# Performance work log

Measured on AMD Instinct MI355X. Metric: run time of the kernel, lower is better.

The kernel has to match this reference:

```python
import jax, jax.numpy as jnp
import numpy as np

BETA = 0.9
THRESH = 1.0
SLOPE = 25.0  # fast_sigmoid surrogate slope

@jax.custom_vjp
def spike(x):
    # forward: heaviside(mem - threshold); backward: fast-sigmoid surrogate
    return (x > 0).astype(x.dtype)

def _spike_fwd(x):
    return (x > 0).astype(x.dtype), x

def _spike_bwd(x, g):
    return (g / (SLOPE * jnp.abs(x) + 1.0) ** 2,)

spike.defvjp(_spike_fwd, _spike_bwd)

def lif_step(mem, cur):
    # snntorch Leaky, reset_mechanism='subtract': reset from previous mem (detached)
    reset = jax.lax.stop_gradient((mem > THRESH).astype(cur.dtype))
    mem_new = BETA * mem + cur - reset * THRESH
    spk = spike(mem_new - THRESH)
    return spk, mem_new

def setup_inputs() -> dict:
    key = jax.random.key(0)
    ks = jax.random.split(key, 10)
    B, S, T = 256, 8, 25
    A, V, H, E = 512, 512, 256, 128
    a_seq = (jax.random.uniform(ks[0], (B, S, T, A)) < 0.2).astype(jnp.float32)
    v_seq = (jax.random.uniform(ks[1], (B, S, T, V)) < 0.2).astype(jnp.float32)
    def lin(kw, kb, out_d, in_d):
        lim = 1.0 / np.sqrt(in_d)
        W = jax.random.uniform(kw, (out_d, in_d), minval=-lim, maxval=lim, dtype=jnp.float32)
        b = jax.random.uniform(kb, (out_d,), minval=-lim, maxval=lim, dtype=jnp.float32)
        return W, b
    W_a1, b_a1 = lin(ks[2], ks[3], H, A)
    W_a2, b_a2 = lin(ks[4], ks[5], E, H)
    W_v1, b_v1 = lin(ks[6], ks[7], H, V)
    W_v2, b_v2 = lin(ks[8], ks[9], E, H)
    return dict(a_seq=a_seq, v_seq=v_seq, W_a1=W_a1, b_a1=b_a1, W_a2=W_a2, b_a2=b_a2,
                W_v1=W_v1, b_v1=b_v1, W_v2=W_v2, b_v2=b_v2)

def reference(a_seq, v_seq, W_a1, b_a1, W_a2, b_a2, W_v1, b_v1, W_v2, b_v2):
    B, S, T, A = a_seq.shape
    V = v_seq.shape[-1]
    H = W_a1.shape[0]
    E = W_a2.shape[0]
    BS = B * S  # segments are independent -> fold into batch
    a = a_seq.reshape(BS, T, A).transpose(1, 0, 2)  # [T, BS, A]
    v = v_seq.reshape(BS, T, V).transpose(1, 0, 2)  # [T, BS, V]

    def step(carry, xs):
        ma1, ma2, mv1, mv2, _, _ = carry
        at, vt = xs
        spk_a1, ma1 = lif_step(ma1, at @ W_a1.T + b_a1)
        spk_a2, ma2 = lif_step(ma2, spk_a1 @ W_a2.T + b_a2)
        spk_v1, mv1 = lif_step(mv1, vt @ W_v1.T + b_v1)
        spk_v2, mv2 = lif_step(mv2, spk_v1 @ W_v2.T + b_v2)
        return (ma1, ma2, mv1, mv2, spk_a2, spk_v2), None

    z = jnp.zeros
    init = (z((BS, H)), z((BS, E)), z((BS, H)), z((BS, E)), z((BS, E)), z((BS, E)))
    (ma1, ma2, mv1, mv2, spk_a2, spk_v2), _ = jax.lax.scan(step, init, (a, v))
    combined = jnp.concatenate([spk_a2, spk_v2], axis=1)  # [BS, 2E]
    norm = jnp.linalg.norm(combined, axis=1, keepdims=True)
    combined = combined / jnp.maximum(norm, 1e-12)  # F.normalize p=2 dim=1
    embs = combined.reshape(B, S, 2 * E)
    return embs.mean(axis=1)  # [B, 2E]
```

## Files before the change

### kernel.cpp

```cpp
#include <hip/hip_runtime.h>


typedef short bf16x8 __attribute__((ext_vector_type(8)));
typedef float f32x4 __attribute__((ext_vector_type(4)));

#define RBIG 51200

__device__ __forceinline__ void glds16(const void* g, void* l) {
    __builtin_amdgcn_global_load_lds((const __attribute__((address_space(1))) void*)g,
                                     (__attribute__((address_space(3))) void*)l, 16, 0, 0);
}

__global__ void prep_w(const float* __restrict__ Wa1, const float* __restrict__ Wv1,
                       const float* __restrict__ Wa2, const float* __restrict__ Wv2,
                       unsigned short* __restrict__ W1s, unsigned short* __restrict__ W2s) {
    int idx = blockIdx.x * 256 + threadIdx.x;
    float w;
    unsigned short* dst;
    int K, k;
    if (idx < 262144) {
        int p = idx >> 17, rem = idx & 131071;
        int n = rem >> 9; k = rem & 511; K = 512;
        const float* src = p ? Wv1 : Wa1;
        w = src[(size_t)n * 512 + k];
        dst = W1s + (size_t)p * 256 * 1536 + (size_t)n * 1536;
    } else {
        int j = idx - 262144;
        int p = j >> 15, rem = j & 32767;
        int n = rem >> 8; k = rem & 255; K = 256;
        const float* src = p ? Wv2 : Wa2;
        w = src[(size_t)n * 256 + k];
        dst = W2s + (size_t)p * 128 * 768 + (size_t)n * 768;
    }
    unsigned int u  = __float_as_uint(w);
    unsigned int hi = u & 0xFFFF0000u;
    float r1 = w - __uint_as_float(hi);
    unsigned int mi = __float_as_uint(r1) & 0xFFFF0000u;
    float r2 = r1 - __uint_as_float(mi);
    dst[k]         = (unsigned short)(hi >> 16);
    dst[K + k]     = (unsigned short)(mi >> 16);
    dst[2 * K + k] = (unsigned short)(__float_as_uint(r2) >> 16);
}

template <int KSRC, int NT, int BM, int BN, int NTHR, int WMW, int WNW, int MINW, bool AF32>
__global__ __launch_bounds__(NTHR, MINW) void gemmG(
    const void* __restrict__ A0, const void* __restrict__ A1,
    const unsigned short* __restrict__ Ws, float* __restrict__ C) {
    constexpr int KE     = 3 * KSRC;
    constexpr int NC     = 3 * (KSRC / 64);
    constexpr int MFR    = BM / WMW / 16;
    constexpr int NFR    = BN / WNW / 16;
    constexpr int AESZ   = AF32 ? 4 : 2;
    constexpr int ABYTES = BM * 64 * AESZ;
    constexpr int BBYTES = BN * 64 * 2;
    constexpr int NAG    = ABYTES / 16 / NTHR;
    constexpr int NBG    = BBYTES / 16 / NTHR;

    __shared__ __align__(1024) char lds[2 * ABYTES + 2 * BBYTES];

    const int tid  = threadIdx.x, lane = tid & 63, wave = tid >> 6;
    const int wm   = wave / WNW, wn = wave % WNW;
    const int bx   = blockIdx.x, bz = blockIdx.z;
    const size_t row0 = (size_t)bx * BM;

    const char* Abase = (const char*)(bz ? A1 : A0) + row0 * KSRC * AESZ;
    const char* Bbase = (const char*)Ws + (size_t)bz * NT * KE * 2;

    size_t offA[NAG];
    int dA[NAG];
#pragma unroll
    for (int j = 0; j < NAG; ++j) {
        int G = tid + j * NTHR;
        int row, sl;
        if constexpr (AF32) { row = G >> 4; sl = G & 15; }
        else                { row = G >> 3; sl = G & 7; }
        offA[j] = (size_t)row * KSRC * AESZ + (size_t)((sl ^ (row & 7)) << 4);
        dA[j]   = wave * 1024 + j * NTHR * 16;
    }
    size_t offB[NBG];
    int dB[NBG];
#pragma unroll
    for (int j = 0; j < NBG; ++j) {
        int G = tid + j * NTHR;
        int n = G >> 3, sl = G & 7;
        offB[j] = (size_t)n * KE * 2 + (size_t)((sl ^ (n & 7)) << 4);
        dB[j]   = wave * 1024 + j * NTHR * 16;
    }

    auto stageA = [&](int kb) {
        const char* s = Abase + (size_t)kb * 64 * AESZ;
        char* d = lds + (kb & 1) * ABYTES;
#pragma unroll
        for (int j = 0; j < NAG; ++j) glds16(s + offA[j], d + dA[j]);
    };
    auto stageB = [&](int kb, int sh, int buf) {
        const char* s = Bbase + ((size_t)sh * KSRC + (size_t)kb * 64) * 2;
        char* d = lds + 2 * ABYTES + buf * BBYTES;
#pragma unroll
        for (int j = 0; j < NBG; ++j) glds16(s + offB[j], d + dB[j]);
    };

    f32x4 acc[MFR][NFR];
    f32x4 zz = {0.f, 0.f, 0.f, 0.f};
#pragma unroll
    for (int i = 0; i < MFR; ++i)
#pragma unroll
        for (int j = 0; j < NFR; ++j) acc[i][j] = zz;

    stageA(0);
    stageB(0, 0, 0);
    __syncthreads();

    const int rfr = lane & 15;
    int kb = 0, s = 0;
    for (int c = 0; c < NC; ++c) {
        int s1 = (s == 2) ? 0 : s + 1;
        int kb1 = (s1 == 0) ? kb + 1 : kb;
        if (c + 1 < NC) {
            stageB(kb1, s1, (c + 1) & 1);
            if (s1 == 0) stageA(kb1);
        }

        const char* Ab = lds + (kb & 1) * ABYTES;
        const unsigned short* Bb = (const unsigned short*)(lds + 2 * ABYTES + (c & 1) * BBYTES);
#pragma unroll
        for (int ks = 0; ks < 2; ++ks) {
            const int kbase = ks * 32 + ((lane >> 4) << 3);
            bf16x8 bb[NFR];
#pragma unroll
            for (int ni = 0; ni < NFR; ++ni) {
                int n = wn * (BN / WNW) + ni * 16 + rfr;
                bb[ni] = *(const bf16x8*)&Bb[(n * 64 + kbase) ^ ((n & 7) << 3)];
            }
#pragma unroll
            for (int mi = 0; mi < MFR; ++mi) {
                int r = wm * (BM / WMW) + mi * 16 + rfr;
                bf16x8 av;
                if constexpr (AF32) {
                    const float* Af = (const float*)Ab;
                    int e1 = (r * 64 + kbase) ^ ((r & 7) << 2);
                    uint4 ua = *(const uint4*)&Af[e1];
                    uint4 ub = *(const uint4*)&Af[e1 ^ 4];
                    uint4 w;
                    w.x = (ua.y & 0xFFFF0000u) | (ua.x >> 16);
                    w.y = (ua.w & 0xFFFF0000u) | (ua.z >> 16);
                    w.z = (ub.y & 0xFFFF0000u) | (ub.x >> 16);
                    w.w = (ub.w & 0xFFFF0000u) | (ub.z >> 16);
                    av = __builtin_bit_cast(bf16x8, w);
                } else {
                    const unsigned short* Au = (const unsigned short*)Ab;
                    av = *(const bf16x8*)&Au[(r * 64 + kbase) ^ ((r & 7) << 3)];
                }
#pragma unroll
                for (int ni = 0; ni < NFR; ++ni)
                    acc[mi][ni] = __builtin_amdgcn_mfma_f32_16x16x32_bf16(
                        av, bb[ni], acc[mi][ni], 0, 0, 0);
            }
        }
        __syncthreads();
        kb = kb1; s = s1;
    }

    float* Cp = C + (size_t)bz * RBIG * NT;
    int r4 = ((lane >> 4) << 2), cl = lane & 15;
#pragma unroll
    for (int mi = 0; mi < MFR; ++mi)
#pragma unroll
        for (int ni = 0; ni < NFR; ++ni) {
            size_t col = (size_t)wn * (BN / WNW) + ni * 16 + cl;
#pragma unroll
            for (int j = 0; j < 4; ++j) {
                size_t row = row0 + wm * (BM / WMW) + mi * 16 + r4 + j;
                Cp[row * NT + col] = acc[mi][ni][j];
            }
        }
}

__global__ void lif1_k(const float* __restrict__ cur, const float* __restrict__ ba1,
                       const float* __restrict__ bv1, unsigned int* __restrict__ spk) {
    int r = blockIdx.x, p = blockIdx.y, d = threadIdx.x;
    const float* c0 = cur + ((size_t)p * RBIG + (size_t)r * 25) * 256 + 2 * d;
    const float* bias = p ? bv1 : ba1;
    float b0 = bias[2 * d], b1 = bias[2 * d + 1];
    float2 cv[25];
#pragma unroll
    for (int t = 0; t < 25; ++t) cv[t] = *(const float2*)(c0 + (size_t)t * 256);
    unsigned int* sp = spk + ((size_t)p * RBIG + (size_t)r * 25) * 128 + d;
    float m0 = 0.f, m1 = 0.f;
#pragma unroll
    for (int t = 0; t < 25; ++t) {
        float r0 = (m0 > 1.f) ? 1.f : 0.f;
        float r1 = (m1 > 1.f) ? 1.f : 0.f;
        m0 = 0.9f * m0 + (cv[t].x + b0) - r0;
        m1 = 0.9f * m1 + (cv[t].y + b1) - r1;
        unsigned int w = (m0 > 1.f ? 0x3F80u : 0u) | (m1 > 1.f ? 0x3F800000u : 0u);
        sp[(size_t)t * 128] = w;
    }
}

__global__ void tail_k(const float* __restrict__ cur2, const float* __restrict__ ba2,
                       const float* __restrict__ bv2, float* __restrict__ out) {
    int b = blockIdx.x, d = threadIdx.x;
    int p = d >> 7, e = d & 127;
    const float* bias = p ? bv2 : ba2;
    float bo = bias[e];
    __shared__ float part[4];
    float acc = 0.f;
    for (int s = 0; s < 8; ++s) {
        int r = b * 8 + s;
        const float* c0 = cur2 + ((size_t)p * RBIG + (size_t)r * 25) * 128 + e;
        float cv[25];
#pragma unroll
        for (int t = 0; t < 25; ++t) cv[t] = c0[(size_t)t * 128];
        float m = 0.f;
#pragma unroll
        for (int t = 0; t < 25; ++t) {
            float rs = (m > 1.f) ? 1.f : 0.f;
            m = 0.9f * m + (cv[t] + bo) - rs;
        }
        float v = (m > 1.f) ? 1.f : 0.f;
        float sq = v;
#pragma unroll
        for (int off = 32; off > 0; off >>= 1) sq += __shfl_down(sq, off);
        if ((d & 63) == 0) part[d >> 6] = sq;
        __syncthreads();
        float nrm = sqrtf(part[0] + part[1] + part[2] + part[3]);
        acc += v / fmaxf(nrm, 1e-12f);
        __syncthreads();
    }
    out[(size_t)b * 256 + d] = acc * 0.125f;
}

extern "C" void kernel_launch(void* const* d_in, const int* in_sizes, int n_in,
                              void* d_out, int out_size, void* d_ws, size_t ws_size,
                              hipStream_t stream) {
    const float* a_seq = (const float*)d_in[0];
    const float* v_seq = (const float*)d_in[1];
    const float* W_a1  = (const float*)d_in[2];
    const float* b_a1  = (const float*)d_in[3];
    const float* W_a2  = (const float*)d_in[4];
    const float* b_a2  = (const float*)d_in[5];
    const float* W_v1  = (const float*)d_in[6];
    const float* b_v1  = (const float*)d_in[7];
    const float* W_v2  = (const float*)d_in[8];
    const float* b_v2  = (const float*)d_in[9];

    char* ws = (char*)d_ws;
    unsigned short* W1s  = (unsigned short*)(ws);
    unsigned short* W2s  = (unsigned short*)(ws + 1572864);
    unsigned short* spk1 = (unsigned short*)(ws + 1966080);
    float*          curb = (float*)(ws + 54394880);
    float*          out  = (float*)d_out;

    prep_w<<<1280, 256, 0, stream>>>(W_a1, W_v1, W_a2, W_v2, W1s, W2s);

    gemmG<512, 256, 128, 256, 512, 2, 4, 2, true>
        <<<dim3(400, 1, 2), 512, 0, stream>>>(a_seq, v_seq, W1s, curb);
    lif1_k<<<dim3(2048, 2), 128, 0, stream>>>(curb, b_a1, b_v1, (unsigned int*)spk1);

    gemmG<256, 128, 64, 128, 256, 2, 2, 3, false>
        <<<dim3(800, 1, 2), 256, 0, stream>>>(
        spk1, spk1 + (size_t)RBIG * 256, W2s, curb);

    tail_k<<<256, 256, 0, stream>>>(curb, b_a2, b_v2, out);
}
```

Measured before the change: 421.8 us.

## Replace double-buffered GEMM with single-buffered 256-thread kernel and XCD-swizzled grid

Rewrites the split-bf16 GEMM as a single-buffered 256-thread kernel with a flattened 1D grid. Block IDs are remapped round-robin across the 8 XCD chiplets so that neighbouring tiles land on the same die, and the first GEMM's N is split into two 128-wide tiles, giving more, smaller blocks. The aim is higher occupancy and better L2 locality. In exchange it drops the load/compute overlap from double buffering, adds two barriers per k-step, and the first GEMM now reads each fp32 A tile twice.

```diff
diff --git a/kernel.cpp b/kernel.cpp
--- a/kernel.cpp
+++ b/kernel.cpp
@@ -42,62 +42,57 @@
     dst[2 * K + k] = (unsigned short)(__float_as_uint(r2) >> 16);
 }
 
-template <int KSRC, int NT, int BM, int BN, int NTHR, int WMW, int WNW, int MINW, bool AF32>
-__global__ __launch_bounds__(NTHR, MINW) void gemmG(
+template <int KSRC, int NT, int BM, int BN, int MINW, bool AF32>
+__global__ __launch_bounds__(256, MINW) void gemmS(
     const void* __restrict__ A0, const void* __restrict__ A1,
     const unsigned short* __restrict__ Ws, float* __restrict__ C) {
-    constexpr int KE     = 3 * KSRC;
-    constexpr int NC     = 3 * (KSRC / 64);
-    constexpr int MFR    = BM / WMW / 16;
-    constexpr int NFR    = BN / WNW / 16;
-    constexpr int AESZ   = AF32 ? 4 : 2;
-    constexpr int ABYTES = BM * 64 * AESZ;
-    constexpr int BBYTES = BN * 64 * 2;
-    constexpr int NAG    = ABYTES / 16 / NTHR;
-    constexpr int NBG    = BBYTES / 16 / NTHR;
-
-    __shared__ __align__(1024) char lds[2 * ABYTES + 2 * BBYTES];
+    constexpr int KE   = 3 * KSRC;
+    constexpr int NKB  = KSRC / 64;
+    constexpr int MFR  = BM / 2 / 16;
+    constexpr int NFR  = BN / 2 / 16;
+    constexpr int AESZ = AF32 ? 4 : 2;
+    constexpr int NBY  = NT / BN;
+    constexpr int NAG  = BM * 64 * AESZ / 16 / 256;
+    constexpr int NBG  = BN * 64 * 2 / 16 / 256;
+    constexpr int GPRA = 64 * AESZ / 16;
+
+    __shared__ __align__(1024) char Al[BM * 64 * AESZ];
+    __shared__ __align__(1024) unsigned short Bl[BN * 64];
 
     const int tid  = threadIdx.x, lane = tid & 63, wave = tid >> 6;
-    const int wm   = wave / WNW, wn = wave % WNW;
-    const int bx   = blockIdx.x, bz = blockIdx.z;
+    const int wm   = wave >> 1, wn = wave & 1;
+
+    const int nwg = gridDim.x;
+    const int orig = blockIdx.x;
+    const int lid = (orig & 7) * (nwg >> 3) + (orig >> 3);
+    const int by = lid % NBY;
+    const int t0 = lid / NBY;
+    const int bz = t0 & 1;
+    const int bx = t0 >> 1;
     const size_t row0 = (size_t)bx * BM;
 
     const char* Abase = (const char*)(bz ? A1 : A0) + row0 * KSRC * AESZ;
-    const char* Bbase = (const char*)Ws + (size_t)bz * NT * KE * 2;
-
-    size_t offA[NAG];
-    int dA[NAG];
-#pragma unroll
-    for (int j = 0; j < NAG; ++j) {
-        int G = tid + j * NTHR;
-        int row, sl;
-        if constexpr (AF32) { row = G >> 4; sl = G & 15; }
-        else                { row = G >> 3; sl = G & 7; }
-        offA[j] = (size_t)row * KSRC * AESZ + (size_t)((sl ^ (row & 7)) << 4);
-        dA[j]   = wave * 1024 + j * NTHR * 16;
-    }
-    size_t offB[NBG];
-    int dB[NBG];
-#pragma unroll
-    for (int j = 0; j < NBG; ++j) {
-        int G = tid + j * NTHR;
-        int n = G >> 3, sl = G & 7;
-        offB[j] = (size_t)n * KE * 2 + (size_t)((sl ^ (n & 7)) << 4);
-        dB[j]   = wave * 1024 + j * NTHR * 16;
-    }
+    const char* Bbase = (const char*)Ws + ((size_t)bz * NT + (size_t)by * BN) * KE * 2;
+
+    const int rowA0 = tid / GPRA, slA = tid % GPRA;
+    const size_t offA0 = (size_t)rowA0 * KSRC * AESZ + (size_t)((slA ^ (rowA0 & 7)) << 4);
+    const int rowB0 = tid >> 3, slB = tid & 7;
+    const size_t offB0 = (size_t)rowB0 * KE * 2 + (size_t)((slB ^ (rowB0 & 7)) << 4);
+    const int dst0 = wave * 1024;
 
     auto stageA = [&](int kb) {
-        const char* s = Abase + (size_t)kb * 64 * AESZ;
-        char* d = lds + (kb & 1) * ABYTES;
-#pragma unroll
-        for (int j = 0; j < NAG; ++j) glds16(s + offA[j], d + dA[j]);
+        const char* s = Abase + (size_t)kb * 64 * AESZ + offA0;
+        char* d = Al + dst0;
+#pragma unroll
+        for (int j = 0; j < NAG; ++j)
+            glds16(s + (size_t)j * (64 * KSRC), d + j * 4096);
     };
-    auto stageB = [&](int kb, int sh, int buf) {
-        const char* s = Bbase + ((size_t)sh * KSRC + (size_t)kb * 64) * 2;
-        char* d = lds + 2 * ABYTES + buf * BBYTES;
-#pragma unroll
-        for (int j = 0; j < NBG; ++j) glds16(s + offB[j], d + dB[j]);
+    auto stageB = [&](int kb, int sp) {
+        const char* s = Bbase + ((size_t)sp * KSRC + (size_t)kb * 64) * 2 + offB0;
+        char* d = (char*)Bl + dst0;
+#pragma unroll
+        for (int j = 0; j < NBG; ++j)
+            glds16(s + (size_t)j * (64 * KE), d + j * 4096);
     };
 
     f32x4 acc[MFR][NFR];
@@ -107,58 +102,49 @@
 #pragma unroll
         for (int j = 0; j < NFR; ++j) acc[i][j] = zz;
 
-    stageA(0);
-    stageB(0, 0, 0);
-    __syncthreads();
-
     const int rfr = lane & 15;
-    int kb = 0, s = 0;
-    for (int c = 0; c < NC; ++c) {
-        int s1 = (s == 2) ? 0 : s + 1;
-        int kb1 = (s1 == 0) ? kb + 1 : kb;
-        if (c + 1 < NC) {
-            stageB(kb1, s1, (c + 1) & 1);
-            if (s1 == 0) stageA(kb1);
+    for (int kb = 0; kb < NKB; ++kb) {
+#pragma unroll 1
+        for (int s = 0; s < 3; ++s) {
+            if (s == 0) stageA(kb);
+            stageB(kb, s);
+            __syncthreads();
+#pragma unroll
+            for (int ks = 0; ks < 2; ++ks) {
+                const int kbase = ks * 32 + ((lane >> 4) << 3);
+                bf16x8 bb[NFR];
+#pragma unroll
+                for (int ni = 0; ni < NFR; ++ni) {
+                    int n = wn * (BN / 2) + ni * 16 + rfr;
+                    bb[ni] = *(const bf16x8*)&Bl[(n * 64 + kbase) ^ ((n & 7) << 3)];
+                }
+#pragma unroll
+                for (int mi = 0; mi < MFR; ++mi) {
+                    int r = wm * (BM / 2) + mi * 16 + rfr;
+                    bf16x8 av;
+                    if constexpr (AF32) {
+                        const float* Af = (const float*)Al;
+                        int e1 = (r * 64 + kbase) ^ ((r & 7) << 2);
+                        uint4 ua = *(const uint4*)&Af[e1];
+                        uint4 ub = *(const uint4*)&Af[e1 ^ 4];
+                        uint4 w;
+                        w.x = (ua.y & 0xFFFF0000u) | (ua.x >> 16);
+                        w.y = (ua.w & 0xFFFF0000u) | (ua.z >> 16);
+                        w.z = (ub.y & 0xFFFF0000u) | (ub.x >> 16);
+                        w.w = (ub.w & 0xFFFF0000u) | (ub.z >> 16);
+                        av = __builtin_bit_cast(bf16x8, w);
+                    } else {
+                        const unsigned short* Au = (const unsigned short*)Al;
+                        av = *(const bf16x8*)&Au[(r * 64 + kbase) ^ ((r & 7) << 3)];
+                    }
+#pragma unroll
+                    for (int ni = 0; ni < NFR; ++ni)
+                        acc[mi][ni] = __builtin_amdgcn_mfma_f32_16x16x32_bf16(
+                            av, bb[ni], acc[mi][ni], 0, 0, 0);
+                }
+            }
+            __syncthreads();
         }
-
-        const char* Ab = lds + (kb & 1) * ABYTES;
-        const unsigned short* Bb = (const unsigned short*)(lds + 2 * ABYTES + (c & 1) * BBYTES);
-#pragma unroll
-        for (int ks = 0; ks < 2; ++ks) {
-            const int kbase = ks * 32 + ((lane >> 4) << 3);
-            bf16x8 bb[NFR];
-#pragma unroll
-            for (int ni = 0; ni < NFR; ++ni) {
-                int n = wn * (BN / WNW) + ni * 16 + rfr;
-                bb[ni] = *(const bf16x8*)&Bb[(n * 64 + kbase) ^ ((n & 7) << 3)];
-            }
-#pragma unroll
-            for (int mi = 0; mi < MFR; ++mi) {
-                int r = wm * (BM / WMW) + mi * 16 + rfr;
-                bf16x8 av;
-                if constexpr (AF32) {
-                    const float* Af = (const float*)Ab;
-                    int e1 = (r * 64 + kbase) ^ ((r & 7) << 2);
-                    uint4 ua = *(const uint4*)&Af[e1];
-                    uint4 ub = *(const uint4*)&Af[e1 ^ 4];
-                    uint4 w;
-                    w.x = (ua.y & 0xFFFF0000u) | (ua.x >> 16);
-                    w.y = (ua.w & 0xFFFF0000u) | (ua.z >> 16);
-                    w.z = (ub.y & 0xFFFF0000u) | (ub.x >> 16);
-                    w.w = (ub.w & 0xFFFF0000u) | (ub.z >> 16);
-                    av = __builtin_bit_cast(bf16x8, w);
-                } else {
-                    const unsigned short* Au = (const unsigned short*)Ab;
-                    av = *(const bf16x8*)&Au[(r * 64 + kbase) ^ ((r & 7) << 3)];
-                }
-#pragma unroll
-                for (int ni = 0; ni < NFR; ++ni)
-                    acc[mi][ni] = __builtin_amdgcn_mfma_f32_16x16x32_bf16(
-                        av, bb[ni], acc[mi][ni], 0, 0, 0);
-            }
-        }
-        __syncthreads();
-        kb = kb1; s = s1;
     }
 
     float* Cp = C + (size_t)bz * RBIG * NT;
@@ -167,10 +153,10 @@
     for (int mi = 0; mi < MFR; ++mi)
 #pragma unroll
         for (int ni = 0; ni < NFR; ++ni) {
-            size_t col = (size_t)wn * (BN / WNW) + ni * 16 + cl;
+            size_t col = (size_t)by * BN + wn * (BN / 2) + ni * 16 + cl;
 #pragma unroll
             for (int j = 0; j < 4; ++j) {
-                size_t row = row0 + wm * (BM / WMW) + mi * 16 + r4 + j;
+                size_t row = row0 + wm * (BM / 2) + mi * 16 + r4 + j;
                 Cp[row * NT + col] = acc[mi][ni][j];
             }
         }
@@ -254,12 +240,11 @@
 
     prep_w<<<1280, 256, 0, stream>>>(W_a1, W_v1, W_a2, W_v2, W1s, W2s);
 
-    gemmG<512, 256, 128, 256, 512, 2, 4, 2, true>
-        <<<dim3(400, 1, 2), 512, 0, stream>>>(a_seq, v_seq, W1s, curb);
+    gemmS<512, 256, 128, 128, 3, true><<<1600, 256, 0, stream>>>(
+        a_seq, v_seq, W1s, curb);
     lif1_k<<<dim3(2048, 2), 128, 0, stream>>>(curb, b_a1, b_v1, (unsigned int*)spk1);
 
-    gemmG<256, 128, 64, 128, 256, 2, 2, 3, false>
-        <<<dim3(800, 1, 2), 256, 0, stream>>>(
+    gemmS<256, 128, 64, 128, 4, false><<<1600, 256, 0, stream>>>(
         spk1, spk1 + (size_t)RBIG * 256, W2s, curb);
 
     tail_k<<<256, 256, 0, stream>>>(curb, b_a2, b_v2, out);
```

Result: faster. 363.3 us (-13.9%).
